# Optimization experiments

Measured on AMD Instinct MI355X. Metric: run time of the kernel, lower is better.

Reference implementation:

```python
import jax, jax.numpy as jnp
import numpy as np

N_APP = 100000
N_ATTR = 50000
E = 500000
D_IN = 128
D_H = 128
D_OUT = 2


def _sage(h_src, h_dst, src, dst, ew, W_self, W_neigh, b, n_dst):
    # DGL SAGEConv('mean') with edge_weight: m_e = ew_e * h_src[src_e];
    # h_neigh_v = sum_e->v m_e / in_degree(v); out = h_dst@W_self + h_neigh@W_neigh + b
    # (feat_drop=0.2 is identity in eval mode)
    m = h_src[src] * ew[:, None]                                   # [E, d]
    s = jax.ops.segment_sum(m, dst, num_segments=n_dst)            # [n_dst, d]
    deg = jax.ops.segment_sum(jnp.ones_like(ew), dst, num_segments=n_dst)
    h_neigh = s / jnp.maximum(deg, 1.0)[:, None]
    return h_dst @ W_self + h_neigh @ W_neigh + b


def _forward(x_app, x_attr, ew0, ew1, ew2,
             Wself1, Wneigh1, b1, Wself2, Wneigh2, b2, Wc, bc,
             src0, dst0, src1, dst1, src2, dst2):
    # ---- layer 1 (HeteroGraphConv, aggregate='sum' over relations per dst ntype) ----
    h_attr = _sage(x_app, x_attr, src0, dst0, ew0, Wself1[0], Wneigh1[0], b1[0], N_ATTR)
    h_app = (_sage(x_attr, x_app, src1, dst1, ew1, Wself1[1], Wneigh1[1], b1[1], N_APP)
             + _sage(x_app, x_app, src2, dst2, ew2, Wself1[2], Wneigh1[2], b1[2], N_APP))
    h_attr = jax.nn.relu(h_attr)
    h_app = jax.nn.relu(h_app)
    # ---- layer 2 ----
    h_attr2 = _sage(h_app, h_attr, src0, dst0, ew0, Wself2[0], Wneigh2[0], b2[0], N_ATTR)
    h_app2 = (_sage(h_attr, h_app, src1, dst1, ew1, Wself2[1], Wneigh2[1], b2[1], N_APP)
              + _sage(h_app, h_app, src2, dst2, ew2, Wself2[2], Wneigh2[2], b2[2], N_APP))
    del h_attr2  # second layer output on 'attribute' is unused by classify
    # ---- classify on 'application' ----
    return h_app2 @ Wc + bc


def setup_inputs() -> dict:
    key = jax.random.key(0)
    ks = jax.random.split(key, 20)
    sc = 1.0 / np.sqrt(D_H)
    return {
        "x_app": jax.random.normal(ks[0], (N_APP, D_IN), jnp.float32),
        "x_attr": jax.random.normal(ks[1], (N_ATTR, D_IN), jnp.float32),
        "ew0": jax.random.uniform(ks[2], (E,), jnp.float32),
        "ew1": jax.random.uniform(ks[3], (E,), jnp.float32),
        "ew2": jax.random.uniform(ks[4], (E,), jnp.float32),
        "Wself1": jax.random.normal(ks[5], (3, D_IN, D_H), jnp.float32) * sc,
        "Wneigh1": jax.random.normal(ks[6], (3, D_IN, D_H), jnp.float32) * sc,
        "b1": jax.random.normal(ks[7], (3, D_H), jnp.float32) * 0.01,
        "Wself2": jax.random.normal(ks[8], (3, D_H, D_H), jnp.float32) * sc,
        "Wneigh2": jax.random.normal(ks[9], (3, D_H, D_H), jnp.float32) * sc,
        "b2": jax.random.normal(ks[10], (3, D_H), jnp.float32) * 0.01,
        "Wc": jax.random.normal(ks[11], (D_H, D_OUT), jnp.float32) * sc,
        "bc": jax.random.normal(ks[12], (D_OUT,), jnp.float32) * 0.01,
        "src0": jax.random.randint(ks[13], (E,), 0, N_APP, jnp.int32),
        "dst0": jax.random.randint(ks[14], (E,), 0, N_ATTR, jnp.int32),
        "src1": jax.random.randint(ks[15], (E,), 0, N_ATTR, jnp.int32),
        "dst1": jax.random.randint(ks[16], (E,), 0, N_APP, jnp.int32),
        "src2": jax.random.randint(ks[17], (E,), 0, N_APP, jnp.int32),
        "dst2": jax.random.randint(ks[18], (E,), 0, N_APP, jnp.int32),
    }


def reference(x_app, x_attr, ew0, ew1, ew2,
              Wself1, Wneigh1, b1, Wself2, Wneigh2, b2, Wc, bc,
              src0, dst0, src1, dst1, src2, dst2):
    return _forward(x_app, x_attr, ew0, ew1, ew2,
                    Wself1, Wneigh1, b1, Wself2, Wneigh2, b2, Wc, bc,
                    src0, dst0, src1, dst1, src2, dst2)
```

## Files before the change

### kernel.cpp

```cpp
#include <hip/hip_runtime.h>

#define NAPP  100000
#define NATTR 50000
#define NE    500000
#define D     128
#define NTOT  (NATTR + 2 * NAPP)
#define SCHUNK 1024
#define SNB   ((NTOT + SCHUNK - 1) / SCHUNK)
#define EGRID ((NE + 255) / 256)
#define GB_APP  ((NAPP + 63) / 64)
#define GB_ATTR ((NATTR + 63) / 64)
#define ECAP  1024

typedef __attribute__((ext_vector_type(8))) short bfrag;
typedef __attribute__((ext_vector_type(4))) float f32x4;

__device__ __forceinline__ short bf16_rn(float x) {
    union { float f; unsigned u; } a; a.f = x;
    unsigned r = (a.u + 0x7fffu + ((a.u >> 16) & 1u)) >> 16;
    return (short)r;
}
__device__ __forceinline__ float bf16_to_f(short s) {
    union { float f; unsigned u; } a;
    a.u = ((unsigned)(unsigned short)s) << 16;
    return a.f;
}

__device__ __forceinline__ void split2(float x, float y, unsigned& hw, unsigned& lw) {
    union { float f; unsigned u; } ax, ay;
    ax.f = x; ay.f = y;
    unsigned hx = (ax.u + 0x7fffu + ((ax.u >> 16) & 1u)) >> 16;
    unsigned hy = (ay.u + 0x7fffu + ((ay.u >> 16) & 1u)) >> 16;
    union { unsigned u; float f; } fx, fy;
    fx.u = hx << 16; fy.u = hy << 16;
    union { float f; unsigned u; } rx, ry;
    rx.f = x - fx.f; ry.f = y - fy.f;
    unsigned lx = (rx.u + 0x7fffu + ((rx.u >> 16) & 1u)) >> 16;
    unsigned ly = (ry.u + 0x7fffu + ((ry.u >> 16) & 1u)) >> 16;
    hw = (hy << 16) | (hx & 0xffffu);
    lw = (ly << 16) | (lx & 0xffffu);
}

__global__ __launch_bounds__(256) void hist3_kernel(
        const int* __restrict__ d0, const int* __restrict__ d1, const int* __restrict__ d2,
        int* __restrict__ h0, int* __restrict__ h1, int* __restrict__ h2) {
    int b = blockIdx.x;
    int rel = b / EGRID;
    int i = (b - rel * EGRID) * 256 + threadIdx.x;
    if (i >= NE) return;
    const int* dst = (rel == 0) ? d0 : (rel == 1) ? d1 : d2;
    int* h = (rel == 0) ? h0 : (rel == 1) ? h1 : h2;
    atomicAdd(&h[dst[i]], 1);
}

__global__ __launch_bounds__(256) void scan_partial_kernel(const int* __restrict__ cur,
                                                           int* __restrict__ bsum) {
    int b = blockIdx.x, t = threadIdx.x;
    int4 v = *((const int4*)(cur + b * SCHUNK) + t);
    int s = v.x + v.y + v.z + v.w;
    __shared__ int sd[256];
    sd[t] = s;
    __syncthreads();
    for (int off = 128; off > 0; off >>= 1) {
        if (t < off) sd[t] += sd[t + off];
        __syncthreads();
    }
    if (t == 0) bsum[b] = sd[0];
}

__global__ __launch_bounds__(256) void scan_offsets_kernel(const int* __restrict__ bsum,
        int* __restrict__ boff, int* __restrict__ rp0, int* __restrict__ rp1,
        int* __restrict__ rp2) {
    int t = threadIdx.x;
    int v = (t < SNB) ? bsum[t] : 0;
    __shared__ int sd[256];
    sd[t] = v;
    __syncthreads();
    for (int off = 1; off < 256; off <<= 1) {
        int u = (t >= off) ? sd[t - off] : 0;
        __syncthreads();
        sd[t] += u;
        __syncthreads();
    }
    boff[t] = sd[t] - v;
    if (t == 0) { rp0[NATTR] = NE; rp1[NAPP] = NE; rp2[NAPP] = NE; }
}

__global__ __launch_bounds__(256) void scan_final_kernel(int* __restrict__ cur,
        const int* __restrict__ boff, int* __restrict__ rp0, int* __restrict__ rp1,
        int* __restrict__ rp2) {
    int b = blockIdx.x, t = threadIdx.x;
    int base = b * SCHUNK + t * 4;
    int4 v = *(const int4*)(cur + base);
    int s = v.x + v.y + v.z + v.w;
    __shared__ int sd[256];
    sd[t] = s;
    __syncthreads();
    for (int off = 1; off < 256; off <<= 1) {
        int u = (t >= off) ? sd[t - off] : 0;
        __syncthreads();
        sd[t] += u;
        __syncthreads();
    }
    int pre = boff[b] + sd[t] - s;
    int ex[4];
    ex[0] = pre;
    ex[1] = ex[0] + v.x;
    ex[2] = ex[1] + v.y;
    ex[3] = ex[2] + v.z;
    #pragma unroll
    for (int i = 0; i < 4; i++) {
        int idx = base + i;
        if (idx < NTOT) {
            int* rp; int loc; int rbase;
            if (idx < NATTR)             { rp = rp0; loc = idx;                 rbase = 0; }
            else if (idx < NATTR + NAPP) { rp = rp1; loc = idx - NATTR;        rbase = NE; }
            else                         { rp = rp2; loc = idx - NATTR - NAPP; rbase = 2 * NE; }
            int val = ex[i] - rbase;
            rp[loc] = val;
            cur[idx] = val;
        }
    }
}

__global__ __launch_bounds__(256) void scatter3_kernel(
        const int* __restrict__ s0, const int* __restrict__ d0, const float* __restrict__ e0,
        int* __restrict__ c0, int2* __restrict__ cw0,
        const int* __restrict__ s1, const int* __restrict__ d1, const float* __restrict__ e1,
        int* __restrict__ c1, int2* __restrict__ cw1,
        const int* __restrict__ s2, const int* __restrict__ d2, const float* __restrict__ e2,
        int* __restrict__ c2, int2* __restrict__ cw2) {
    int b = blockIdx.x;
    int rel = b / EGRID;
    int i = (b - rel * EGRID) * 256 + threadIdx.x;
    if (i >= NE) return;
    const int* src; const int* dst; const float* ew; int* cur; int2* cw;
    if (rel == 0)      { src = s0; dst = d0; ew = e0; cur = c0; cw = cw0; }
    else if (rel == 1) { src = s1; dst = d1; ew = e1; cur = c1; cw = cw1; }
    else               { src = s2; dst = d2; ew = e2; cur = c2; cw = cw2; }
    int p = atomicAdd(&cur[dst[i]], 1);
    int2 v;
    v.x = src[i];
    v.y = __float_as_int(ew[i]);
    cw[p] = v;
}

__global__ __launch_bounds__(256) void pack_kernel(
        const float* __restrict__ Wself1, const float* __restrict__ Wneigh1,
        const float* __restrict__ Wself2, const float* __restrict__ Wneigh2,
        const float* __restrict__ b1, const float* __restrict__ b2,
        const float* __restrict__ Wc, const float* __restrict__ bc,
        short* __restrict__ PBh, short* __restrict__ PBl,
        float* __restrict__ b1s, float* __restrict__ b2s,
        float* __restrict__ Cs, float* __restrict__ C1, float* __restrict__ C2,
        float* __restrict__ bconst) {
    int m = blockIdx.x;
    if (m == 8) {
        int tid = threadIdx.x;
        int k = tid >> 1, j = tid & 1;
        const float* Wn1 = Wneigh2 + D * D;
        const float* Wn2 = Wneigh2 + 2 * D * D;
        const float* Ws1 = Wself2 + D * D;
        const float* Ws2 = Wself2 + 2 * D * D;
        float ss = 0.f, s1 = 0.f, s2 = 0.f;
        for (int tt = 0; tt < D; tt++) {
            float wc = Wc[tt * 2 + j];
            ss += (Ws1[k * D + tt] + Ws2[k * D + tt]) * wc;
            s1 += Wn1[k * D + tt] * wc;
            s2 += Wn2[k * D + tt] * wc;
        }
        Cs[tid] = ss; C1[tid] = s1; C2[tid] = s2;
        if (tid < 2) {
            float s = bc[tid];
            for (int tt = 0; tt < D; tt++)
                s += (b2[D + tt] + b2[2 * D + tt]) * Wc[tt * 2 + tid];
            bconst[tid] = s;
        }
        return;
    }
    const float* srcA; const float* srcB = nullptr;
    switch (m) {
        case 0: srcA = Wself1; break;
        case 1: srcA = Wneigh1; break;
        case 2: srcA = Wself1 + D * D; srcB = Wself1 + 2 * D * D; break;
        case 3: srcA = Wneigh1 + D * D; break;
        case 4: srcA = Wneigh1 + 2 * D * D; break;
        case 5: srcA = Wself2 + D * D; srcB = Wself2 + 2 * D * D; break;
        case 6: srcA = Wneigh2 + D * D; break;
        default: srcA = Wneigh2 + 2 * D * D; break;
    }
    short* oh = PBh + (size_t)m * D * D;
    short* ol = PBl + (size_t)m * D * D;
    for (int i = threadIdx.x; i < D * D; i += 256) {
        int k = i >> 7, n = i & 127;
        float v = srcA[i];
        if (srcB) v += srcB[i];
        short hi = bf16_rn(v);
        short lo = bf16_rn(v - bf16_to_f(hi));
        int kc = k >> 5, q = (k >> 3) & 3, j = k & 7, nt = n >> 4, c = n & 15;
        int pos = (((kc * 8 + nt) * 64) + q * 16 + c) * 8 + j;
        oh[pos] = hi;
        ol[pos] = lo;
    }
    if (m == 0 && threadIdx.x < D) {
        int t = threadIdx.x;
        b1s[t] = b1[D + t] + b1[2 * D + t];
        b2s[t] = b2[D + t] + b2[2 * D + t];
    }
}

#define ASTR 128
template<int NG>
__device__ __forceinline__ void fused_body(
        const float* __restrict__ in0, const short* __restrict__ B0h, const short* __restrict__ B0l,
        const float* __restrict__ x1, const int* __restrict__ rp1, const int2* __restrict__ cw1,
        const short* __restrict__ B1h, const short* __restrict__ B1l,
        const float* __restrict__ x2, const int* __restrict__ rp2, const int2* __restrict__ cw2,
        const short* __restrict__ B2h, const short* __restrict__ B2l,
        const float* __restrict__ bias,
        const float* __restrict__ Ccol0, const float* __restrict__ Ccol1,
        float* __restrict__ zo0, float* __restrict__ zo1,
        int nrows, int row0, float* At, int2* eds) {
    const int t = threadIdx.x;
    const int w = t >> 6, lane = t & 63;
    const int q = lane >> 4, c = lane & 15;
    const int myrow = row0 + w * 16 + c;
    const int arow = min(myrow, nrows - 1);

    f32x4 acc[8];
    #pragma unroll
    for (int nt = 0; nt < 8; nt++) acc[nt] = (f32x4){0.f, 0.f, 0.f, 0.f};

    {
        const float* __restrict__ arp = in0 + (size_t)arow * D;
        const bfrag* __restrict__ Bh = (const bfrag*)B0h;
        const bfrag* __restrict__ Bl = (const bfrag*)B0l;
        #pragma unroll
        for (int kc = 0; kc < 4; kc++) {
            float4 a0 = *(const float4*)(arp + kc * 32 + q * 8);
            float4 a1 = *(const float4*)(arp + kc * 32 + q * 8 + 4);
            union { unsigned u[4]; bfrag v; } ahu, alu;
            split2(a0.x, a0.y, ahu.u[0], alu.u[0]);
            split2(a0.z, a0.w, ahu.u[1], alu.u[1]);
            split2(a1.x, a1.y, ahu.u[2], alu.u[2]);
            split2(a1.z, a1.w, ahu.u[3], alu.u[3]);
            bfrag ah = ahu.v, al = alu.v;
            const bfrag* bh = Bh + kc * 512 + lane;
            const bfrag* bl = Bl + kc * 512 + lane;
            #pragma unroll
            for (int nt = 0; nt < 8; nt++) {
                bfrag vh = bh[nt * 64];
                bfrag vl = bl[nt * 64];
                acc[nt] = __builtin_amdgcn_mfma_f32_16x16x32_bf16(ah, vh, acc[nt], 0, 0, 0);
                acc[nt] = __builtin_amdgcn_mfma_f32_16x16x32_bf16(ah, vl, acc[nt], 0, 0, 0);
                acc[nt] = __builtin_amdgcn_mfma_f32_16x16x32_bf16(al, vh, acc[nt], 0, 0, 0);
            }
        }
    }

    const int grp = t >> 5, l32 = t & 31;
    #pragma unroll
    for (int g = 0; g < NG; g++) {
        const float* __restrict__ xs = (g == 0) ? x1 : x2;
        const int* __restrict__ rp   = (g == 0) ? rp1 : rp2;
        const int2* __restrict__ cw  = (g == 0) ? cw1 : cw2;
        const short* __restrict__ Bhp = (g == 0) ? B1h : B2h;
        const short* __restrict__ Blp = (g == 0) ? B1l : B2l;

        if (g > 0) __syncthreads();
        const int eb0 = rp[row0];
        const int eb1 = rp[min(row0 + 64, nrows)];
        const int ecnt = eb1 - eb0;
        const bool staged = (ecnt < ECAP);
        if (staged) {
            for (int i = t; i < ecnt; i += 256) eds[i] = cw[eb0 + i];
            if (t == 0) eds[ecnt] = make_int2(0, 0);
        }
        __syncthreads();

        {
            const int r0g = row0 + grp * 8;
            int bnd[9];
            #pragma unroll
            for (int i = 0; i < 9; i++) bnd[i] = rp[min(r0g + i, nrows)];
            #pragma unroll
            for (int p = 0; p < 4; p++) {
                const int A0 = bnd[2 * p],     A1 = bnd[2 * p + 1];
                const int B0 = bnd[2 * p + 1], B1 = bnd[2 * p + 2];
                float4 aA = make_float4(0.f, 0.f, 0.f, 0.f);
                float4 aB = make_float4(0.f, 0.f, 0.f, 0.f);
                const int lastA = min(max(A1 - 1, A0), NE - 1);
                const int lastB = min(max(B1 - 1, B0), NE - 1);
                int jA = A0, jB = B0;
                while (jA < A1 || jB < B1) {
                    int2 ed[8];
                    if (staged) {
                        #pragma unroll
                        for (int u = 0; u < 4; u++)
                            ed[u] = eds[min(min(jA + u, lastA) - eb0, ecnt)];
                        #pragma unroll
                        for (int u = 0; u < 4; u++)
                            ed[4 + u] = eds[min(min(jB + u, lastB) - eb0, ecnt)];
                    } else {
                        #pragma unroll
                        for (int u = 0; u < 4; u++) ed[u] = cw[min(jA + u, lastA)];
                        #pragma unroll
                        for (int u = 0; u < 4; u++) ed[4 + u] = cw[min(jB + u, lastB)];
                    }
                    float wt[8];
                    #pragma unroll
                    for (int u = 0; u < 4; u++)
                        wt[u] = (jA + u < A1) ? __int_as_float(ed[u].y) : 0.f;
                    #pragma unroll
                    for (int u = 0; u < 4; u++)
                        wt[4 + u] = (jB + u < B1) ? __int_as_float(ed[4 + u].y) : 0.f;
                    float4 v[8];
                    #pragma unroll
                    for (int u = 0; u < 8; u++)
                        v[u] = *(const float4*)(xs + (size_t)ed[u].x * D + l32 * 4);
                    aA.x += wt[0] * v[0].x + wt[1] * v[1].x + wt[2] * v[2].x + wt[3] * v[3].x;
                    aA.y += wt[0] * v[0].y + wt[1] * v[1].y + wt[2] * v[2].y + wt[3] * v[3].y;
                    aA.z += wt[0] * v[0].z + wt[1] * v[1].z + wt[2] * v[2].z + wt[3] * v[3].z;
                    aA.w += wt[0] * v[0].w + wt[1] * v[1].w + wt[2] * v[2].w + wt[3] * v[3].w;
                    aB.x += wt[4] * v[4].x + wt[5] * v[5].x + wt[6] * v[6].x + wt[7] * v[7].x;
                    aB.y += wt[4] * v[4].y + wt[5] * v[5].y + wt[6] * v[6].y + wt[7] * v[7].y;
                    aB.z += wt[4] * v[4].z + wt[5] * v[5].z + wt[6] * v[6].z + wt[7] * v[7].z;
                    aB.w += wt[4] * v[4].w + wt[5] * v[5].w + wt[6] * v[6].w + wt[7] * v[7].w;
                    jA += 4; jB += 4;
                }
                const float invA = 1.0f / (float)max(A1 - A0, 1);
                const float invB = 1.0f / (float)max(B1 - B0, 1);
                aA.x *= invA; aA.y *= invA; aA.z *= invA; aA.w *= invA;
                aB.x *= invB; aB.y *= invB; aB.z *= invB; aB.w *= invB;
                const int lrA = grp * 8 + 2 * p;
                const int lrB = lrA + 1;
                *(float4*)&At[lrA * ASTR + ((l32 ^ ((lrA & 3) << 1)) << 2)] = aA;
                *(float4*)&At[lrB * ASTR + ((l32 ^ ((lrB & 3) << 1)) << 2)] = aB;
            }
        }
        __syncthreads();

        const bfrag* __restrict__ Bh = (const bfrag*)Bhp;
        const bfrag* __restrict__ Bl = (const bfrag*)Blp;
        const int rloc = w * 16 + c;
        const int sw = (rloc & 3) << 1;
        const float* __restrict__ arow_lds = &At[rloc * ASTR];
        #pragma unroll
        for (int kc = 0; kc < 4; kc++) {
            const int g0 = kc * 8 + q * 2;
            float4 a0 = *(const float4*)(arow_lds + ((g0 ^ sw) << 2));
            float4 a1 = *(const float4*)(arow_lds + (((g0 + 1) ^ sw) << 2));
            union { unsigned u[4]; bfrag v; } ahu, alu;
            split2(a0.x, a0.y, ahu.u[0], alu.u[0]);
            split2(a0.z, a0.w, ahu.u[1], alu.u[1]);
            split2(a1.x, a1.y, ahu.u[2], alu.u[2]);
            split2(a1.z, a1.w, ahu.u[3], alu.u[3]);
            bfrag ah = ahu.v, al = alu.v;
            const bfrag* bh = Bh + kc * 512 + lane;
            const bfrag* bl = Bl + kc * 512 + lane;
            #pragma unroll
            for (int nt = 0; nt < 8; nt++) {
                bfrag vh = bh[nt * 64];
                bfrag vl = bl[nt * 64];
                acc[nt] = __builtin_amdgcn_mfma_f32_16x16x32_bf16(ah, vh, acc[nt], 0, 0, 0);
                acc[nt] = __builtin_amdgcn_mfma_f32_16x16x32_bf16(ah, vl, acc[nt], 0, 0, 0);
                acc[nt] = __builtin_amdgcn_mfma_f32_16x16x32_bf16(al, vh, acc[nt], 0, 0, 0);
            }
        }
    }

    float c00[8], c01[8], c10[8], c11[8], bvv[8];
    #pragma unroll
    for (int nt = 0; nt < 8; nt++) {
        float2 v0 = *(const float2*)(Ccol0 + (nt * 16 + c) * 2);
        c00[nt] = v0.x; c01[nt] = v0.y;
        if (NG == 2) {
            float2 v1 = *(const float2*)(Ccol1 + (nt * 16 + c) * 2);
            c10[nt] = v1.x; c11[nt] = v1.y;
        }
        bvv[nt] = bias[nt * 16 + c];
    }
    #pragma unroll
    for (int r = 0; r < 4; r++) {
        int row = row0 + w * 16 + q * 4 + r;
        float s0 = 0.f, s1 = 0.f, t0 = 0.f, t1 = 0.f;
        #pragma unroll
        for (int nt = 0; nt < 8; nt++) {
            float h = fmaxf(acc[nt][r] + bvv[nt], 0.f);
            s0 += h * c00[nt]; s1 += h * c01[nt];
            if (NG == 2) { t0 += h * c10[nt]; t1 += h * c11[nt]; }
        }
        #pragma unroll
        for (int off = 1; off < 16; off <<= 1) {
            s0 += __shfl_xor(s0, off);
            s1 += __shfl_xor(s1, off);
            if (NG == 2) { t0 += __shfl_xor(t0, off); t1 += __shfl_xor(t1, off); }
        }
        if (c == 0 && row < nrows) {
            *(float2*)(zo0 + (size_t)row * 2) = make_float2(s0, s1);
            if (NG == 2) *(float2*)(zo1 + (size_t)row * 2) = make_float2(t0, t1);
        }
    }
}

__global__ __launch_bounds__(256, 4) void fused_all_kernel(
        const float* __restrict__ xapp, const float* __restrict__ xattr,
        const short* __restrict__ PBh, const short* __restrict__ PBl,
        const int* __restrict__ rp0, const int2* __restrict__ cw0,
        const int* __restrict__ rp1, const int2* __restrict__ cw1,
        const int* __restrict__ rp2, const int2* __restrict__ cw2,
        const float* __restrict__ b1, const float* __restrict__ b1s,
        const float* __restrict__ Cs, const float* __restrict__ C2,
        const float* __restrict__ C1,
        float* __restrict__ zs, float* __restrict__ z2, float* __restrict__ za) {
    __shared__ __align__(16) float At[64 * ASTR];
    __shared__ __align__(16) int2 eds[ECAP];
    const size_t MM = (size_t)D * D;
    int b = blockIdx.x;
    if (b < GB_APP) {
        fused_body<2>(xapp, PBh + 2 * MM, PBl + 2 * MM,
                      xattr, rp1, cw1, PBh + 3 * MM, PBl + 3 * MM,
                      xapp,  rp2, cw2, PBh + 4 * MM, PBl + 4 * MM,
                      b1s, Cs, C2, zs, z2, NAPP, b * 64, At, eds);
    } else {
        int bb = b - GB_APP;
        fused_body<1>(xattr, PBh, PBl,
                      xapp, rp0, cw0, PBh + 1 * MM, PBl + 1 * MM,
                      nullptr, nullptr, nullptr, nullptr, nullptr,
                      b1, C1, nullptr, za, nullptr, NATTR, bb * 64, At, eds);
    }
}

__global__ __launch_bounds__(256) void final_out_kernel(
        const float* __restrict__ zs, const float* __restrict__ za,
        const float* __restrict__ z2,
        const int* __restrict__ rp1, const int2* __restrict__ cw1,
        const int* __restrict__ rp2, const int2* __restrict__ cw2,
        const float* __restrict__ bconst, float* __restrict__ out, int n) {
    int r = (blockIdx.x * 256 + threadIdx.x) >> 3;
    int l = threadIdx.x & 7;
    if (r >= n) return;
    int s0 = rp1[r], s1 = rp1[r + 1];
    float q0 = 0.f, q1 = 0.f;
    for (int j = s0 + l; j < s1; j += 8) {
        int2 e = cw1[j];
        float w = __int_as_float(e.y);
        float2 v = *(const float2*)(za + (size_t)e.x * 2);
        q0 += w * v.x; q1 += w * v.y;
    }
    float inv1 = 1.0f / (float)max(s1 - s0, 1);
    float p0 = q0 * inv1, p1 = q1 * inv1;
    s0 = rp2[r]; s1 = rp2[r + 1];
    q0 = 0.f; q1 = 0.f;
    for (int j = s0 + l; j < s1; j += 8) {
        int2 e = cw2[j];
        float w = __int_as_float(e.y);
        float2 v = *(const float2*)(z2 + (size_t)e.x * 2);
        q0 += w * v.x; q1 += w * v.y;
    }
    float inv2 = 1.0f / (float)max(s1 - s0, 1);
    p0 += q0 * inv2; p1 += q1 * inv2;
    #pragma unroll
    for (int off = 1; off < 8; off <<= 1) {
        p0 += __shfl_xor(p0, off);
        p1 += __shfl_xor(p1, off);
    }
    if (l == 0) {
        float2 s = *(const float2*)(zs + (size_t)r * 2);
        out[(size_t)r * 2 + 0] = p0 + s.x + bconst[0];
        out[(size_t)r * 2 + 1] = p1 + s.y + bconst[1];
    }
}

extern "C" void kernel_launch(void* const* d_in, const int* in_sizes, int n_in,
                              void* d_out, int out_size, void* d_ws, size_t ws_size,
                              hipStream_t stream) {
    const float* x_app   = (const float*)d_in[0];
    const float* x_attr  = (const float*)d_in[1];
    const float* ew0     = (const float*)d_in[2];
    const float* ew1     = (const float*)d_in[3];
    const float* ew2     = (const float*)d_in[4];
    const float* Wself1  = (const float*)d_in[5];
    const float* Wneigh1 = (const float*)d_in[6];
    const float* b1      = (const float*)d_in[7];
    const float* Wself2  = (const float*)d_in[8];
    const float* Wneigh2 = (const float*)d_in[9];
    const float* b2      = (const float*)d_in[10];
    const float* Wc      = (const float*)d_in[11];
    const float* bc      = (const float*)d_in[12];
    const int* src0 = (const int*)d_in[13];
    const int* dst0 = (const int*)d_in[14];
    const int* src1 = (const int*)d_in[15];
    const int* dst1 = (const int*)d_in[16];
    const int* src2 = (const int*)d_in[17];
    const int* dst2 = (const int*)d_in[18];
    float* out = (float*)d_out;

    float* ws = (float*)d_ws;
    float* h_attr = ws;
    float* h_app  = h_attr + (size_t)NATTR * D;
    float* b1s    = h_app  + (size_t)NAPP * D;
    float* b2s    = b1s + D;
    float* za     = b2s + D;
    float* zsv    = za + (size_t)NATTR * 2;
    float* z2v    = zsv + (size_t)NAPP * 2;
    float* Cs     = z2v + (size_t)NAPP * 2;
    float* C1     = Cs + 256;
    float* C2     = C1 + 256;
    float* bconst = C2 + 256;
    int* cur  = (int*)(bconst + 4);
    int* cur0 = cur;
    int* cur1 = cur0 + NATTR;
    int* cur2 = cur1 + NAPP;
    int* rp0  = cur + SNB * SCHUNK;
    int* rp1  = rp0 + NATTR + 4;
    int* rp2  = rp1 + NAPP + 4;
    int* bsum = rp2 + NAPP + 4;
    int* boff = bsum + 256;
    int2* cw0 = (int2*)(boff + 256);
    int2* cw1 = cw0 + NE;
    int2* cw2 = cw1 + NE;
    short* PBh = (short*)(cw2 + NE);
    short* PBl = PBh + (size_t)8 * D * D;

    hipMemsetAsync(cur, 0, (size_t)SNB * SCHUNK * sizeof(int), stream);

    pack_kernel<<<9, 256, 0, stream>>>(Wself1, Wneigh1, Wself2, Wneigh2,
                                       b1, b2, Wc, bc, PBh, PBl, b1s, b2s,
                                       Cs, C1, C2, bconst);

    hist3_kernel<<<3 * EGRID, 256, 0, stream>>>(dst0, dst1, dst2, cur0, cur1, cur2);
    scan_partial_kernel<<<SNB, 256, 0, stream>>>(cur, bsum);
    scan_offsets_kernel<<<1, 256, 0, stream>>>(bsum, boff, rp0, rp1, rp2);
    scan_final_kernel<<<SNB, 256, 0, stream>>>(cur, boff, rp0, rp1, rp2);
    scatter3_kernel<<<3 * EGRID, 256, 0, stream>>>(
        src0, dst0, ew0, cur0, cw0,
        src1, dst1, ew1, cur1, cw1,
        src2, dst2, ew2, cur2, cw2);

    fused_all_kernel<<<GB_APP + GB_ATTR, 256, 0, stream>>>(
        x_app, x_attr, PBh, PBl,
        rp0, cw0, rp1, cw1, rp2, cw2,
        b1, b1s, Cs, C2, C1, zsv, z2v, za);

    final_out_kernel<<<((size_t)NAPP * 8 + 255) / 256, 256, 0, stream>>>(
        zsv, za, z2v, rp1, cw1, rp2, cw2, bconst, out, NAPP);
}
```

Before: 490.4 us.

## Record per-edge ranks in histogram pass to make CSR scatter atomic-free

The histogram kernel now stores the slot returned by each atomicAdd as a per-edge rank, and the scatter kernel places each edge at rp[dst]+rank without a second round of atomics. Both kernels process four edges per thread with vectorized int4/float4 loads, and scan_final no longer rewrites the cursor array. The final output kernel uses 4 lanes per row instead of 8. This trades a second atomic pass for an extra 6 MB rank buffer (aliased onto h_attr workspace) written and read once.

```diff
diff --git a/kernel.cpp b/kernel.cpp
--- a/kernel.cpp
+++ b/kernel.cpp
@@ -7,7 +7,7 @@
 #define NTOT  (NATTR + 2 * NAPP)
 #define SCHUNK 1024
 #define SNB   ((NTOT + SCHUNK - 1) / SCHUNK)
-#define EGRID ((NE + 255) / 256)
+#define EG4   ((NE / 4 + 255) / 256)
 #define GB_APP  ((NAPP + 63) / 64)
 #define GB_ATTR ((NATTR + 63) / 64)
 #define ECAP  1024
@@ -43,14 +43,22 @@
 
 __global__ __launch_bounds__(256) void hist3_kernel(
         const int* __restrict__ d0, const int* __restrict__ d1, const int* __restrict__ d2,
-        int* __restrict__ h0, int* __restrict__ h1, int* __restrict__ h2) {
+        int* __restrict__ h0, int* __restrict__ h1, int* __restrict__ h2,
+        int* __restrict__ r0, int* __restrict__ r1, int* __restrict__ r2) {
     int b = blockIdx.x;
-    int rel = b / EGRID;
-    int i = (b - rel * EGRID) * 256 + threadIdx.x;
-    if (i >= NE) return;
+    int rel = b / EG4;
+    int i4 = (b - rel * EG4) * 256 + threadIdx.x;
+    if (i4 * 4 >= NE) return;
     const int* dst = (rel == 0) ? d0 : (rel == 1) ? d1 : d2;
     int* h = (rel == 0) ? h0 : (rel == 1) ? h1 : h2;
-    atomicAdd(&h[dst[i]], 1);
+    int* rk = (rel == 0) ? r0 : (rel == 1) ? r1 : r2;
+    int4 d = *((const int4*)dst + i4);
+    int4 r;
+    r.x = atomicAdd(&h[d.x], 1);
+    r.y = atomicAdd(&h[d.y], 1);
+    r.z = atomicAdd(&h[d.z], 1);
+    r.w = atomicAdd(&h[d.w], 1);
+    *((int4*)rk + i4) = r;
 }
 
 __global__ __launch_bounds__(256) void scan_partial_kernel(const int* __restrict__ cur,
@@ -86,7 +94,7 @@
     if (t == 0) { rp0[NATTR] = NE; rp1[NAPP] = NE; rp2[NAPP] = NE; }
 }
 
-__global__ __launch_bounds__(256) void scan_final_kernel(int* __restrict__ cur,
+__global__ __launch_bounds__(256) void scan_final_kernel(const int* __restrict__ cur,
         const int* __restrict__ boff, int* __restrict__ rp0, int* __restrict__ rp1,
         int* __restrict__ rp2) {
     int b = blockIdx.x, t = threadIdx.x;
@@ -116,33 +124,34 @@
             if (idx < NATTR)             { rp = rp0; loc = idx;                 rbase = 0; }
             else if (idx < NATTR + NAPP) { rp = rp1; loc = idx - NATTR;        rbase = NE; }
             else                         { rp = rp2; loc = idx - NATTR - NAPP; rbase = 2 * NE; }
-            int val = ex[i] - rbase;
-            rp[loc] = val;
-            cur[idx] = val;
+            rp[loc] = ex[i] - rbase;
         }
     }
 }
 
 __global__ __launch_bounds__(256) void scatter3_kernel(
         const int* __restrict__ s0, const int* __restrict__ d0, const float* __restrict__ e0,
-        int* __restrict__ c0, int2* __restrict__ cw0,
+        const int* __restrict__ r0, const int* __restrict__ rp0, int2* __restrict__ cw0,
         const int* __restrict__ s1, const int* __restrict__ d1, const float* __restrict__ e1,
-        int* __restrict__ c1, int2* __restrict__ cw1,
+        const int* __restrict__ r1, const int* __restrict__ rp1, int2* __restrict__ cw1,
         const int* __restrict__ s2, const int* __restrict__ d2, const float* __restrict__ e2,
-        int* __restrict__ c2, int2* __restrict__ cw2) {
+        const int* __restrict__ r2, const int* __restrict__ rp2, int2* __restrict__ cw2) {
     int b = blockIdx.x;
-    int rel = b / EGRID;
-    int i = (b - rel * EGRID) * 256 + threadIdx.x;
-    if (i >= NE) return;
-    const int* src; const int* dst; const float* ew; int* cur; int2* cw;
-    if (rel == 0)      { src = s0; dst = d0; ew = e0; cur = c0; cw = cw0; }
-    else if (rel == 1) { src = s1; dst = d1; ew = e1; cur = c1; cw = cw1; }
-    else               { src = s2; dst = d2; ew = e2; cur = c2; cw = cw2; }
-    int p = atomicAdd(&cur[dst[i]], 1);
-    int2 v;
-    v.x = src[i];
-    v.y = __float_as_int(ew[i]);
-    cw[p] = v;
+    int rel = b / EG4;
+    int i4 = (b - rel * EG4) * 256 + threadIdx.x;
+    if (i4 * 4 >= NE) return;
+    const int* src; const int* dst; const float* ew; const int* rk; const int* rp; int2* cw;
+    if (rel == 0)      { src = s0; dst = d0; ew = e0; rk = r0; rp = rp0; cw = cw0; }
+    else if (rel == 1) { src = s1; dst = d1; ew = e1; rk = r1; rp = rp1; cw = cw1; }
+    else               { src = s2; dst = d2; ew = e2; rk = r2; rp = rp2; cw = cw2; }
+    int4 s = *((const int4*)src + i4);
+    int4 d = *((const int4*)dst + i4);
+    float4 e = *((const float4*)ew + i4);
+    int4 r = *((const int4*)rk + i4);
+    cw[rp[d.x] + r.x] = make_int2(s.x, __float_as_int(e.x));
+    cw[rp[d.y] + r.y] = make_int2(s.y, __float_as_int(e.y));
+    cw[rp[d.z] + r.z] = make_int2(s.z, __float_as_int(e.z));
+    cw[rp[d.w] + r.w] = make_int2(s.w, __float_as_int(e.w));
 }
 
 __global__ __launch_bounds__(256) void pack_kernel(
@@ -437,12 +446,12 @@
         const int* __restrict__ rp1, const int2* __restrict__ cw1,
         const int* __restrict__ rp2, const int2* __restrict__ cw2,
         const float* __restrict__ bconst, float* __restrict__ out, int n) {
-    int r = (blockIdx.x * 256 + threadIdx.x) >> 3;
-    int l = threadIdx.x & 7;
+    int r = (blockIdx.x * 256 + threadIdx.x) >> 2;
+    int l = threadIdx.x & 3;
     if (r >= n) return;
     int s0 = rp1[r], s1 = rp1[r + 1];
     float q0 = 0.f, q1 = 0.f;
-    for (int j = s0 + l; j < s1; j += 8) {
+    for (int j = s0 + l; j < s1; j += 4) {
         int2 e = cw1[j];
         float w = __int_as_float(e.y);
         float2 v = *(const float2*)(za + (size_t)e.x * 2);
@@ -452,7 +461,7 @@
     float p0 = q0 * inv1, p1 = q1 * inv1;
     s0 = rp2[r]; s1 = rp2[r + 1];
     q0 = 0.f; q1 = 0.f;
-    for (int j = s0 + l; j < s1; j += 8) {
+    for (int j = s0 + l; j < s1; j += 4) {
         int2 e = cw2[j];
         float w = __int_as_float(e.y);
         float2 v = *(const float2*)(z2 + (size_t)e.x * 2);
@@ -461,7 +470,7 @@
     float inv2 = 1.0f / (float)max(s1 - s0, 1);
     p0 += q0 * inv2; p1 += q1 * inv2;
     #pragma unroll
-    for (int off = 1; off < 8; off <<= 1) {
+    for (int off = 1; off < 4; off <<= 1) {
         p0 += __shfl_xor(p0, off);
         p1 += __shfl_xor(p1, off);
     }
@@ -522,6 +531,9 @@
     int2* cw2 = cw1 + NE;
     short* PBh = (short*)(cw2 + NE);
     short* PBl = PBh + (size_t)8 * D * D;
+    int* rank0 = (int*)h_attr;
+    int* rank1 = rank0 + NE;
+    int* rank2 = rank1 + NE;
 
     hipMemsetAsync(cur, 0, (size_t)SNB * SCHUNK * sizeof(int), stream);
 
@@ -529,20 +541,21 @@
                                        b1, b2, Wc, bc, PBh, PBl, b1s, b2s,
                                        Cs, C1, C2, bconst);
 
-    hist3_kernel<<<3 * EGRID, 256, 0, stream>>>(dst0, dst1, dst2, cur0, cur1, cur2);
+    hist3_kernel<<<3 * EG4, 256, 0, stream>>>(dst0, dst1, dst2, cur0, cur1, cur2,
+                                              rank0, rank1, rank2);
     scan_partial_kernel<<<SNB, 256, 0, stream>>>(cur, bsum);
     scan_offsets_kernel<<<1, 256, 0, stream>>>(bsum, boff, rp0, rp1, rp2);
     scan_final_kernel<<<SNB, 256, 0, stream>>>(cur, boff, rp0, rp1, rp2);
-    scatter3_kernel<<<3 * EGRID, 256, 0, stream>>>(
-        src0, dst0, ew0, cur0, cw0,
-        src1, dst1, ew1, cur1, cw1,
-        src2, dst2, ew2, cur2, cw2);
+    scatter3_kernel<<<3 * EG4, 256, 0, stream>>>(
+        src0, dst0, ew0, rank0, rp0, cw0,
+        src1, dst1, ew1, rank1, rp1, cw1,
+        src2, dst2, ew2, rank2, rp2, cw2);
 
     fused_all_kernel<<<GB_APP + GB_ATTR, 256, 0, stream>>>(
         x_app, x_attr, PBh, PBl,
         rp0, cw0, rp1, cw1, rp2, cw2,
         b1, b1s, Cs, C2, C1, zsv, z2v, za);
 
-    final_out_kernel<<<((size_t)NAPP * 8 + 255) / 256, 256, 0, stream>>>(
+    final_out_kernel<<<((size_t)NAPP * 4 + 255) / 256, 256, 0, stream>>>(
         zsv, za, z2v, rp1, cw1, rp2, cw2, bconst, out, NAPP);
 }
```

Measured after the change: 421.3 us. -14.1%, faster.
